# Kernel optimization log

Hardware: AMD Instinct MI355X
Metric: run time of the kernel (lower is better)

Reference implementation:

```python
import jax, jax.numpy as jnp
import numpy as np

B, T, D, H, L, W = 32, 512, 256, 8, 2, 10
NQ = 10000
HD = D // H


def setup_inputs():
    key = jax.random.key(0)
    ks = jax.random.split(key, 16)
    def n(k, shape, s=0.02):
        return jax.random.normal(k, shape, jnp.float32) * s
    return {
        "q": jax.random.randint(ks[0], (B, T), 0, NQ),
        "s": jax.random.randint(ks[1], (B, T), 0, 2),
        "q_embed": n(ks[2], (NQ + 1, D)),
        "s_embed": n(ks[3], (2, D)),
        "pos_embed": n(ks[4], (512, D)),
        "fusion_w": n(ks[5], (2 * D, D)),
        "fusion_b": jnp.zeros((D,), jnp.float32),
        "in_proj_w": n(ks[6], (L, D, 3 * D)),
        "in_proj_b": jnp.zeros((L, 3 * D), jnp.float32),
        "out_proj_w": n(ks[7], (L, D, D)),
        "out_proj_b": jnp.zeros((L, D), jnp.float32),
        "ln1_g": jnp.ones((L, D), jnp.float32),
        "ln1_b": jnp.zeros((L, D), jnp.float32),
        "ln2_g": jnp.ones((L, D), jnp.float32),
        "ln2_b": jnp.zeros((L, D), jnp.float32),
        "ff1_w": n(ks[8], (L, D, 4 * D)),
        "ff1_b": jnp.zeros((L, 4 * D), jnp.float32),
        "ff2_w": n(ks[9], (L, 4 * D, D)),
        "ff2_b": jnp.zeros((L, D), jnp.float32),
        "sw1": n(ks[10], (6, 32), 0.1),
        "sb1": jnp.zeros((32,), jnp.float32),
        "sw2": n(ks[11], (32, D // 4), 0.1),
        "sb2": jnp.zeros((D // 4,), jnp.float32),
        "cw1": n(ks[12], (D + D // 4, D)),
        "cb1": jnp.zeros((D,), jnp.float32),
        "cw2": n(ks[13], (D, 1)),
        "cb2": jnp.zeros((1,), jnp.float32),
    }


def _ln(x, g, b):
    mu = jnp.mean(x, -1, keepdims=True)
    var = jnp.mean(jnp.square(x - mu), -1, keepdims=True)
    return (x - mu) * jax.lax.rsqrt(var + 1e-5) * g + b


def _sliding_sum(x, w):
    # sum over trailing window of size w ending at each t, via prefix sums
    c = jnp.concatenate([jnp.zeros((x.shape[0], 1), x.dtype), jnp.cumsum(x, axis=1)], axis=1)
    t = jnp.arange(x.shape[1])
    return c[:, t + 1] - c[:, jnp.maximum(t + 1 - w, 0)]


def _stats(s, mask):
    # vectorized version of _extract_statistics (prefix-sum sliding windows)
    mf = mask.astype(jnp.float32)
    sf = s.astype(jnp.float32) * mf
    valid = _sliding_sum(mf, W)
    correct_rate = _sliding_sum(sf, W) / (valid + 1e-6)
    rc = _sliding_sum(mf, 5)
    recent_correct = _sliding_sum(sf, 5) / (rc + 1e-6)
    trans = ((s[:, 1:] != s[:, :-1]) & mask[:, 1:] & mask[:, :-1]).astype(jnp.float32)
    diff = jnp.concatenate([jnp.zeros((s.shape[0], 1), jnp.float32), trans], axis=1)
    change_rate = _sliding_sum(diff, W - 1) / (valid + 1e-6)
    # max consecutive equal run within each trailing window of size W
    sp = jnp.pad(s, ((0, 0), (W - 1, 0)))
    mp = jnp.pad(mask, ((0, 0), (W - 1, 0)))
    win_s = [sp[:, j:j + T] for j in range(W)]
    win_m = [mp[:, j:j + T] for j in range(W)]
    run = win_m[0].astype(jnp.float32)
    mx = run
    for j in range(1, W):  # fixed small window, not a data-dim loop
        eq = (win_s[j] == win_s[j - 1]) & win_m[j - 1]
        run = win_m[j].astype(jnp.float32) * (jnp.where(eq, run, 0.0) + 1.0)
        mx = jnp.maximum(mx, run)
    rel = jnp.broadcast_to(jnp.arange(T, dtype=jnp.float32) / max(T, 100), s.shape)
    cov = valid / W
    return jnp.stack([correct_rate, recent_correct, change_rate, mx / W, rel, cov], axis=-1)


def reference(q, s, q_embed, s_embed, pos_embed, fusion_w, fusion_b, in_proj_w, in_proj_b,
              out_proj_w, out_proj_b, ln1_g, ln1_b, ln2_g, ln2_b, ff1_w, ff1_b, ff2_w, ff2_b,
              sw1, sb1, sw2, sb2, cw1, cb1, cw2, cb2):
    mask = s >= 0
    qm = jnp.where(mask, q, 0)
    sm = jnp.where(mask, s, 0)
    h = jnp.concatenate([q_embed[qm], s_embed[sm]], axis=-1)  # [B,T,2D]
    h = jax.nn.relu(h @ fusion_w + fusion_b) + pos_embed[:T][None]
    causal = jnp.tril(jnp.ones((T, T), bool))
    allowed = causal[None, None] & mask[:, None, None, :]
    scale = 1.0 / (HD ** 0.5)
    for l in range(L):
        qkv = h @ in_proj_w[l] + in_proj_b[l]
        qh, kh, vh = jnp.split(qkv, 3, axis=-1)
        qh = qh.reshape(B, T, H, HD).transpose(0, 2, 1, 3)
        kh = kh.reshape(B, T, H, HD).transpose(0, 2, 1, 3)
        vh = vh.reshape(B, T, H, HD).transpose(0, 2, 1, 3)
        scores = jnp.einsum('bhqd,bhkd->bhqk', qh, kh) * scale
        scores = jnp.where(allowed, scores, -1e9)
        attn = jax.nn.softmax(scores, axis=-1)
        o = jnp.einsum('bhqk,bhkd->bhqd', attn, vh).transpose(0, 2, 1, 3).reshape(B, T, D)
        h = _ln(h + (o @ out_proj_w[l] + out_proj_b[l]), ln1_g[l], ln1_b[l])
        ff = jax.nn.gelu(h @ ff1_w[l] + ff1_b[l], approximate=False) @ ff2_w[l] + ff2_b[l]
        h = _ln(h + ff, ln2_g[l], ln2_b[l])
    sfeat = _stats(sm, mask)  # [B,T,6]
    semb = jax.nn.relu(sfeat @ sw1 + sb1) @ sw2 + sb2  # [B,T,D//4]
    comb = jnp.concatenate([h, semb], axis=-1)
    logits = (jax.nn.relu(comb @ cw1 + cb1) @ cw2 + cb2)[..., 0]
    return jnp.where(mask, logits, -1e9)
```

## Files before the change

kernel.cpp:

```cpp
#include <hip/hip_runtime.h>
#include <hip/hip_bf16.h>
#include <cmath>


using short8 = __attribute__((ext_vector_type(8))) short;
using short4v = __attribute__((ext_vector_type(4))) short;
using f32x4  = __attribute__((ext_vector_type(4))) float;

__device__ inline float gelu_f(float x) {
    return 0.5f * x * (1.0f + erff(x * 0.70710678118654752f));
}

__device__ inline short f2bf(float x) {
    union { float f; unsigned u; } v; v.f = x;
    return (short)((v.u + 0x7fffu + ((v.u >> 16) & 1u)) >> 16);
}

__device__ inline float bf2f(short v) {
    union { unsigned u; float f; } x; x.u = ((unsigned)(unsigned short)v) << 16;
    return x.f;
}

__device__ inline unsigned packbf(float lo, float hi) {
    union { float f; unsigned u; } a, b; a.f = lo; b.f = hi;
    unsigned ra = (a.u + 0x7fffu + ((a.u >> 16) & 1u)) >> 16;
    unsigned rb = (b.u + 0x7fffu + ((b.u >> 16) & 1u)) >> 16;
    return (rb << 16) | (ra & 0xffffu);
}

#define GLOAD16(gp, lp) __builtin_amdgcn_global_load_lds( \
    (const __attribute__((address_space(1))) void*)(gp), \
    (__attribute__((address_space(3))) void*)(lp), 16, 0, 0)

__global__ __launch_bounds__(256) void prep(
    const float* __restrict__ fusion_w, const float* __restrict__ in_proj_w,
    const float* __restrict__ out_proj_w, const float* __restrict__ ff1_w,
    const float* __restrict__ ff2_w, const float* __restrict__ cw1,
    short* __restrict__ wts,
    const int* __restrict__ s,
    short* __restrict__ semb,
    const float* __restrict__ sw1, const float* __restrict__ sb1,
    const float* __restrict__ sw2, const float* __restrict__ sb2)
{
    __shared__ float tile[4][32][33];
    __shared__ float sv_sh[512];
    __shared__ float m_sh[512];
    __shared__ float sw2_sh[2048];

    if (blockIdx.x < 436) {
        const int b0[10]      = {0,128,320,512,576,640,896,1152,1408,1664};
        const int Ks[10]      = {512,256,256,256,256,256,256,1024,1024,320};
        const int Ns[10]      = {256,768,768,256,256,1024,1024,256,256,256};
        const int sidx[10]    = {0,1,1,2,2,3,3,4,4,5};
        const size_t soff[10] = {0,0,196608,0,65536,0,262144,0,262144,0};
        const size_t doff[10] = {0,131072,327680,524288,589824,655360,917504,1179648,1441792,1703936};
        const float* srcs[6] = {fusion_w, in_proj_w, out_proj_w, ff1_w, ff2_w, cw1};
        const int c = threadIdx.x & 31, r = threadIdx.x >> 5;

        int mis[4], txs[4], tys[4];
#pragma unroll
        for (int i = 0; i < 4; ++i) {
            int tg = blockIdx.x * 4 + i;
            int mi = 0;
            while (mi < 9 && tg >= b0[mi + 1]) ++mi;
            int bl = tg - b0[mi];
            mis[i] = mi;
            txs[i] = bl % (Ns[mi] >> 5);
            tys[i] = bl / (Ns[mi] >> 5);
        }
#pragma unroll
        for (int i = 0; i < 4; ++i) {
            const float* src = srcs[sidx[mis[i]]] + soff[mis[i]];
            const int N = Ns[mis[i]];
#pragma unroll
            for (int u = 0; u < 4; ++u)
                tile[i][r + u * 8][c] =
                    src[(size_t)(tys[i] * 32 + r + u * 8) * N + txs[i] * 32 + c];
        }
        __syncthreads();
#pragma unroll
        for (int i = 0; i < 4; ++i) {
            short* dst = wts + doff[mis[i]];
            const int K = Ks[mis[i]];
#pragma unroll
            for (int u = 0; u < 4; ++u)
                dst[(size_t)(txs[i] * 32 + r + u * 8) * K + tys[i] * 32 + c] =
                    f2bf(tile[i][c][r + u * 8]);
        }
    } else {
        const int b = blockIdx.x - 436;
        const int tt = threadIdx.x;
        for (int t = tt; t < 512; t += 256) {
            int sval = s[b * 512 + t];
            bool mk = sval >= 0;
            sv_sh[t] = mk ? (float)sval : 0.f;
            m_sh[t] = mk ? 1.f : 0.f;
        }
        for (int i = tt; i < 2048; i += 256) sw2_sh[i] = sw2[i];
        __syncthreads();
        for (int half = 0; half < 2; ++half) {
            const int t = tt + half * 256;
            float mf10 = 0, sf10 = 0, mf5 = 0, sf5 = 0, d9 = 0;
#pragma unroll
            for (int k = 0; k < 10; ++k) {
                int idx = t - k;
                if (idx >= 0) {
                    float mv = m_sh[idx], sv = sv_sh[idx];
                    mf10 += mv; sf10 += sv;
                    if (k < 5) { mf5 += mv; sf5 += sv; }
                    if (k < 9 && idx >= 1) {
                        if (sv != sv_sh[idx - 1] && mv > 0.5f && m_sh[idx - 1] > 0.5f) d9 += 1.f;
                    }
                }
            }
            float run, mx;
            {
                int x0 = t - 9;
                run = (x0 >= 0) ? m_sh[x0] : 0.f;
                mx = run;
#pragma unroll
                for (int j = 1; j < 10; ++j) {
                    int xc = t + j - 9, xp = xc - 1;
                    float sc = (xc >= 0) ? sv_sh[xc] : 0.f;
                    float sp = (xp >= 0) ? sv_sh[xp] : 0.f;
                    float mc = (xc >= 0) ? m_sh[xc] : 0.f;
                    float mp = (xp >= 0) ? m_sh[xp] : 0.f;
                    bool eq = (sc == sp) && (mp > 0.5f);
                    run = (mc > 0.5f) ? ((eq ? run : 0.f) + 1.f) : 0.f;
                    mx = fmaxf(mx, run);
                }
            }
            float f[6];
            f[0] = sf10 / (mf10 + 1e-6f);
            f[1] = sf5 / (mf5 + 1e-6f);
            f[2] = d9 / (mf10 + 1e-6f);
            f[3] = mx * 0.1f;
            f[4] = (float)t * (1.f / 512.f);
            f[5] = mf10 * 0.1f;

            float hid[32];
#pragma unroll
            for (int j2 = 0; j2 < 32; ++j2) {
                float a = sb1[j2];
#pragma unroll
                for (int i = 0; i < 6; ++i) a = fmaf(f[i], sw1[i * 32 + j2], a);
                hid[j2] = fmaxf(a, 0.f);
            }
            short* orow = semb + ((size_t)b * 512 + t) * 64;
            for (int c = 0; c < 64; c += 4) {
                float v0 = sb2[c], v1 = sb2[c + 1], v2 = sb2[c + 2], v3 = sb2[c + 3];
#pragma unroll
                for (int j2 = 0; j2 < 32; ++j2) {
                    float hh = hid[j2];
                    v0 = fmaf(hh, sw2_sh[j2 * 64 + c], v0);
                    v1 = fmaf(hh, sw2_sh[j2 * 64 + c + 1], v1);
                    v2 = fmaf(hh, sw2_sh[j2 * 64 + c + 2], v2);
                    v3 = fmaf(hh, sw2_sh[j2 * 64 + c + 3], v3);
                }
                short4v o; o[0] = f2bf(v0); o[1] = f2bf(v1); o[2] = f2bf(v2); o[3] = f2bf(v3);
                *(short4v*)(orow + c) = o;
            }
        }
    }
}

template<int EPI, int KTOT>
__global__ __launch_bounds__(512) void kbs(
    const short* __restrict__ A, const short* __restrict__ Wt,
    const float* __restrict__ bias,
    short* __restrict__ o0, short* __restrict__ o1, short* __restrict__ o2,
    const float* __restrict__ pos,
    const int* __restrict__ qi, const int* __restrict__ si,
    const float* __restrict__ qe, const float* __restrict__ se)
{
    constexpr int BN = 64;
    constexpr int NCH = (KTOT + 255) / 256;
    __shared__ short Bs[BN * 256];
    const int tid = threadIdx.x, lane = tid & 63, wv = tid >> 6;
    const int lg = lane >> 4, lr = lane & 15;
    const int n0 = blockIdx.y * BN;
    const int row0 = blockIdx.x * 128 + wv * 16;

    f32x4 acc[4] = {};
    short8 af[8];

#pragma unroll
    for (int c = 0; c < NCH; ++c) {
        const int ck = (KTOT - c * 256 >= 256) ? 256 : (KTOT - c * 256);
        const int spr = ck >> 3;
        if (c) __syncthreads();
        for (int i = 0; i < (BN * ck) / 8; i += 512) {
            int slot = i + tid;
            int n = slot / spr, posn = slot % spr;
            int g = posn ^ (n & 7);
            GLOAD16(Wt + (size_t)(n0 + n) * KTOT + c * 256 + g * 8, &Bs[slot * 8]);
        }
        const int nkk = ck >> 5;
        if constexpr (EPI == 0) {
            int row = row0 + lr;
            int sv = si[row];
            bool mk = sv >= 0;
            const float* base = (c == 0) ? qe + (size_t)(mk ? qi[row] : 0) * 256
                                         : se + (size_t)(mk ? sv : 0) * 256;
#pragma unroll
            for (int kk = 0; kk < 8; ++kk) {
                const float* p = base + kk * 32 + lg * 8;
                float4 v0 = *(const float4*)p;
                float4 v1 = *(const float4*)(p + 4);
                short8 o;
                o[0] = f2bf(v0.x); o[1] = f2bf(v0.y); o[2] = f2bf(v0.z); o[3] = f2bf(v0.w);
                o[4] = f2bf(v1.x); o[5] = f2bf(v1.y); o[6] = f2bf(v1.z); o[7] = f2bf(v1.w);
                af[kk] = o;
            }
        } else {
            const short* ar = A + (size_t)(row0 + lr) * KTOT + c * 256 + lg * 8;
#pragma unroll
            for (int kk = 0; kk < 8; ++kk)
                if (kk < nkk) af[kk] = *(const short8*)(ar + kk * 32);
        }
        __syncthreads();
#pragma unroll
        for (int kk = 0; kk < 8; ++kk) {
            if (kk >= nkk) break;
#pragma unroll
            for (int j = 0; j < 4; ++j) {
                int n = j * 16 + lr;
                short8 b = *(const short8*)&Bs[n * ck + (((kk * 4 + lg) ^ (n & 7)) << 3)];
                acc[j] = __builtin_amdgcn_mfma_f32_16x16x32_bf16(af[kk], b, acc[j], 0, 0, 0);
            }
        }
    }

    if constexpr (EPI == 0) {
#pragma unroll
        for (int j = 0; j < 4; ++j)
#pragma unroll
        for (int r = 0; r < 4; ++r) {
            int row = row0 + lg * 4 + r;
            int col = n0 + j * 16 + lr;
            float x = acc[j][r] + bias[col];
            x = fmaxf(x, 0.f) + pos[(size_t)(row & 511) * 256 + col];
            o0[(size_t)row * 256 + col] = f2bf(x);
        }
    } else if constexpr (EPI == 1) {
#pragma unroll
        for (int j = 0; j < 4; ++j)
#pragma unroll
        for (int r = 0; r < 4; ++r) {
            int row = row0 + lg * 4 + r;
            int gcol = n0 + j * 16 + lr;
            int t = row & 511, bg = row >> 9;
            int sec = gcol >> 8, cc = gcol & 255;
            int h = cc >> 5, d = cc & 31, bh = bg * 8 + h;
            short v = f2bf(acc[j][r] + bias[gcol]);
            if (sec == 0)      o0[((size_t)bh * 512 + t) * 32 + d] = v;
            else if (sec == 1) o1[((size_t)bh * 512 + t) * 32 + d] = v;
            else {
                int kl = t & 31;
                o2[(size_t)bh * 16384 + (size_t)(t >> 5) * 1024 +
                   (size_t)((kl >> 2) & 3) * 256 + d * 8 + (((kl & 3) << 1) | ((kl >> 4) & 1))] = v;
            }
        }
    } else {
#pragma unroll
        for (int j = 0; j < 4; ++j)
#pragma unroll
        for (int r = 0; r < 4; ++r) {
            int row = row0 + lg * 4 + r;
            int gcol = n0 + j * 16 + lr;
            float x = acc[j][r] + bias[gcol];
            o0[(size_t)row * 1024 + gcol] = f2bf(gelu_f(x));
        }
    }
}

template<int EPI, int KTOT>
__global__ __launch_bounds__(512) void kfull(
    const short* __restrict__ A, const short* __restrict__ A2,
    const short* __restrict__ Wt, const float* __restrict__ bias,
    short* __restrict__ hb,
    const float* __restrict__ gamma, const float* __restrict__ beta,
    const float* __restrict__ cw2v, const float* __restrict__ cb2,
    const int* __restrict__ smask, float* __restrict__ outlog)
{
    constexpr int NCH = (KTOT + 127) / 128;
    constexpr int KA = (EPI == 1) ? 256 : KTOT;
    __shared__ short Bs[256 * 128];
    __shared__ float redS[32][4];
    __shared__ float redQ[32][4];
    const int tid = threadIdx.x, lane = tid & 63, wv = tid >> 6;
    const int lg = lane >> 4, lr = lane & 15;
    const int wr = wv >> 2, wc = wv & 3;
    const int row0 = blockIdx.x * 32 + wr * 16;

    f32x4 acc[4] = {};
    short8 af[4];

#pragma unroll
    for (int c = 0; c < NCH; ++c) {
        const int ck = (KTOT - c * 128 >= 128) ? 128 : (KTOT - c * 128);
        const int spr = ck >> 3;
        if (c) __syncthreads();
        for (int i = 0; i < (256 * ck) / 8; i += 512) {
            int slot = i + tid;
            int n = slot / spr, posn = slot % spr;
            int g = posn ^ (n & 7);
            GLOAD16(Wt + (size_t)n * KTOT + c * 128 + g * 8, &Bs[slot * 8]);
        }
        const int nkk = ck >> 5;
        if (EPI == 1 && c == 2) {
            const short* ar2 = A2 + (size_t)(row0 + lr) * 64 + lg * 8;
            af[0] = *(const short8*)(ar2);
            af[1] = *(const short8*)(ar2 + 32);
        } else {
            const short* ar = A + (size_t)(row0 + lr) * KA + c * 128 + lg * 8;
#pragma unroll
            for (int kk = 0; kk < 4; ++kk)
                if (kk < nkk) af[kk] = *(const short8*)(ar + kk * 32);
        }
        __syncthreads();
#pragma unroll
        for (int kk = 0; kk < 4; ++kk) {
            if (kk >= nkk) break;
#pragma unroll
            for (int j = 0; j < 4; ++j) {
                int n = wc * 64 + j * 16 + lr;
                short8 b = *(const short8*)&Bs[n * ck + (((kk * 4 + lg) ^ (n & 7)) << 3)];
                acc[j] = __builtin_amdgcn_mfma_f32_16x16x32_bf16(af[kk], b, acc[j], 0, 0, 0);
            }
        }
    }

    if constexpr (EPI == 0) {
        float ps[4] = {0.f, 0.f, 0.f, 0.f}, pq[4] = {0.f, 0.f, 0.f, 0.f};
#pragma unroll
        for (int j = 0; j < 4; ++j)
#pragma unroll
        for (int r = 0; r < 4; ++r) {
            int row = row0 + lg * 4 + r;
            int col = wc * 64 + j * 16 + lr;
            float x = acc[j][r] + bias[col] + bf2f(hb[(size_t)row * 256 + col]);
            acc[j][r] = x;
            ps[r] += x; pq[r] += x * x;
        }
#pragma unroll
        for (int off = 1; off < 16; off <<= 1)
#pragma unroll
            for (int r = 0; r < 4; ++r) {
                ps[r] += __shfl_xor(ps[r], off);
                pq[r] += __shfl_xor(pq[r], off);
            }
        if (lr == 0) {
#pragma unroll
            for (int r = 0; r < 4; ++r) {
                int rl = wr * 16 + lg * 4 + r;
                redS[rl][wc] = ps[r]; redQ[rl][wc] = pq[r];
            }
        }
        __syncthreads();
#pragma unroll
        for (int r = 0; r < 4; ++r) {
            int rl = wr * 16 + lg * 4 + r;
            int row = row0 + lg * 4 + r;
            float sm = redS[rl][0] + redS[rl][1] + redS[rl][2] + redS[rl][3];
            float sq = redQ[rl][0] + redQ[rl][1] + redQ[rl][2] + redQ[rl][3];
            float mu = sm * (1.f / 256.f);
            float var = sq * (1.f / 256.f) - mu * mu;
            float rstd = rsqrtf(var + 1e-5f);
#pragma unroll
            for (int j = 0; j < 4; ++j) {
                int col = wc * 64 + j * 16 + lr;
                float y = (acc[j][r] - mu) * rstd * gamma[col] + beta[col];
                hb[(size_t)row * 256 + col] = f2bf(y);
            }
        }
    } else {
        float p[4] = {0.f, 0.f, 0.f, 0.f};
#pragma unroll
        for (int j = 0; j < 4; ++j)
#pragma unroll
        for (int r = 0; r < 4; ++r) {
            int col = wc * 64 + j * 16 + lr;
            float v = fmaxf(acc[j][r] + bias[col], 0.f);
            p[r] += v * cw2v[col];
        }
#pragma unroll
        for (int off = 1; off < 16; off <<= 1)
#pragma unroll
            for (int r = 0; r < 4; ++r) p[r] += __shfl_xor(p[r], off);
        if (lr == 0) {
#pragma unroll
            for (int r = 0; r < 4; ++r)
                redS[wr * 16 + lg * 4 + r][wc] = p[r];
        }
        __syncthreads();
        if (tid < 32) {
            int row = blockIdx.x * 32 + tid;
            float v = redS[tid][0] + redS[tid][1] + redS[tid][2] + redS[tid][3] + cb2[0];
            outlog[row] = (smask[row] >= 0) ? v : -1e9f;
        }
    }
}

__global__ __launch_bounds__(256) void attn_mfma(
    const short* __restrict__ Qg, const short* __restrict__ Kg,
    const short* __restrict__ VTg, short* __restrict__ O)
{
    __shared__ unsigned Wp[4][2][16][20];
    const int bh = blockIdx.x >> 2, part = blockIdx.x & 3;
    const int b = bh >> 3, h = bh & 7;
    const int wv = threadIdx.x >> 6, lane = threadIdx.x & 63;
    const int lg = lane >> 4, lr = lane & 15;
    const int slot = part * 4 + wv;
    const short* Qbh = Qg + (size_t)bh * 16384;
    const short* Kbh = Kg + (size_t)bh * 16384;
    const short* Vbh = VTg + (size_t)bh * 16384;
    const float scale = 0.17677669529663687f;

    const int tA = slot, tB = 31 - slot;
    const int qA0 = tA << 4, qB0 = tB << 4;
    const int nA = tA >> 1, nB = tB >> 1;
    short8 qaA = *(const short8*)(Qbh + (size_t)(qA0 + lr) * 32 + lg * 8);
    short8 qaB = *(const short8*)(Qbh + (size_t)(qB0 + lr) * 32 + lg * 8);
    f32x4 oA0 = {}, oA1 = {}, oB0 = {}, oB1 = {};
    float lA[4] = {0.f, 0.f, 0.f, 0.f};
    float lB[4] = {0.f, 0.f, 0.f, 0.f};

    auto chunk = [&](int c, int q0, int nfull, const short8& qa,
                     const short8& kf0, const short8& kf1,
                     const short8& vf0, const short8& vf1,
                     f32x4& o0, f32x4& o1, float* l_, int slab) {
        int kc = c << 5;
        f32x4 s0 = {}, s1 = {};
        s0 = __builtin_amdgcn_mfma_f32_16x16x32_bf16(qa, kf0, s0, 0, 0, 0);
        s1 = __builtin_amdgcn_mfma_f32_16x16x32_bf16(qa, kf1, s1, 0, 0, 0);
        float p0[4], p1[4];
        if (c < nfull) {
#pragma unroll
            for (int r = 0; r < 4; ++r) {
                p0[r] = __expf(s0[r] * scale);
                p1[r] = __expf(s1[r] * scale);
            }
        } else {
#pragma unroll
            for (int r = 0; r < 4; ++r) {
                int qq = q0 + lg * 4 + r;
                p0[r] = (kc + lr)      > qq ? 0.f : __expf(s0[r] * scale);
                p1[r] = (kc + 16 + lr) > qq ? 0.f : __expf(s1[r] * scale);
            }
        }
#pragma unroll
        for (int r = 0; r < 4; ++r) {
            l_[r] += p0[r] + p1[r];
            Wp[wv][slab][lg * 4 + r][lr] = packbf(p0[r], p1[r]);
        }
        short8 pa = *(const short8*)&Wp[wv][slab][lr][lg * 4];
        o0 = __builtin_amdgcn_mfma_f32_16x16x32_bf16(pa, vf0, o0, 0, 0, 0);
        o1 = __builtin_amdgcn_mfma_f32_16x16x32_bf16(pa, vf1, o1, 0, 0, 0);
    };

    int c = 0;
    for (; c <= nA; ++c) {
        int kc = c << 5;
        short8 kf0 = *(const short8*)(Kbh + (size_t)(kc + lr) * 32 + lg * 8);
        short8 kf1 = *(const short8*)(Kbh + (size_t)(kc + 16 + lr) * 32 + lg * 8);
        short8 vf0 = *(const short8*)(Vbh + (size_t)c * 1024 + lg * 256 + lr * 8);
        short8 vf1 = *(const short8*)(Vbh + (size_t)c * 1024 + lg * 256 + (lr + 16) * 8);
        chunk(c, qB0, nB, qaB, kf0, kf1, vf0, vf1, oB0, oB1, lB, 1);
        chunk(c, qA0, nA, qaA, kf0, kf1, vf0, vf1, oA0, oA1, lA, 0);
    }
    for (; c <= nB; ++c) {
        int kc = c << 5;
        short8 kf0 = *(const short8*)(Kbh + (size_t)(kc + lr) * 32 + lg * 8);
        short8 kf1 = *(const short8*)(Kbh + (size_t)(kc + 16 + lr) * 32 + lg * 8);
        short8 vf0 = *(const short8*)(Vbh + (size_t)c * 1024 + lg * 256 + lr * 8);
        short8 vf1 = *(const short8*)(Vbh + (size_t)c * 1024 + lg * 256 + (lr + 16) * 8);
        chunk(c, qB0, nB, qaB, kf0, kf1, vf0, vf1, oB0, oB1, lB, 1);
    }

#pragma unroll
    for (int off = 1; off < 16; off <<= 1)
#pragma unroll
        for (int r = 0; r < 4; ++r) {
            lA[r] += __shfl_xor(lA[r], off);
            lB[r] += __shfl_xor(lB[r], off);
        }
#pragma unroll
    for (int r = 0; r < 4; ++r) {
        float invA = 1.f / lA[r];
        size_t roA = ((size_t)b * 512 + qA0 + lg * 4 + r) * 256 + h * 32;
        O[roA + lr] = f2bf(oA0[r] * invA);
        O[roA + 16 + lr] = f2bf(oA1[r] * invA);
        float invB = 1.f / lB[r];
        size_t roB = ((size_t)b * 512 + qB0 + lg * 4 + r) * 256 + h * 32;
        O[roB + lr] = f2bf(oB0[r] * invB);
        O[roB + 16 + lr] = f2bf(oB1[r] * invB);
    }
}

extern "C" void kernel_launch(void* const* d_in, const int* in_sizes, int n_in,
                              void* d_out, int out_size, void* d_ws, size_t ws_size,
                              hipStream_t stream) {
    const int*   q         = (const int*)d_in[0];
    const int*   s         = (const int*)d_in[1];
    const float* q_embed   = (const float*)d_in[2];
    const float* s_embed   = (const float*)d_in[3];
    const float* pos_embed = (const float*)d_in[4];
    const float* fusion_w  = (const float*)d_in[5];
    const float* fusion_b  = (const float*)d_in[6];
    const float* in_proj_w = (const float*)d_in[7];
    const float* in_proj_b = (const float*)d_in[8];
    const float* out_proj_w= (const float*)d_in[9];
    const float* out_proj_b= (const float*)d_in[10];
    const float* ln1_g     = (const float*)d_in[11];
    const float* ln1_b     = (const float*)d_in[12];
    const float* ln2_g     = (const float*)d_in[13];
    const float* ln2_b     = (const float*)d_in[14];
    const float* ff1_w     = (const float*)d_in[15];
    const float* ff1_b     = (const float*)d_in[16];
    const float* ff2_w     = (const float*)d_in[17];
    const float* ff2_b     = (const float*)d_in[18];
    const float* sw1       = (const float*)d_in[19];
    const float* sb1       = (const float*)d_in[20];
    const float* sw2       = (const float*)d_in[21];
    const float* sb2       = (const float*)d_in[22];
    const float* cw1       = (const float*)d_in[23];
    const float* cb1       = (const float*)d_in[24];
    const float* cw2       = (const float*)d_in[25];
    const float* cb2       = (const float*)d_in[26];
    float* out = (float*)d_out;

    char* base = (char*)d_ws;
    short* hb   = (short*)(base);
    short* bufA = (short*)(base + 8388608);
    short* att  = (short*)(base + 41943040);
    short* Qg   = (short*)(base + 50331648);
    short* Kg   = (short*)(base + 58720256);
    short* VTg  = (short*)(base + 67108864);
    short* semb = (short*)(base + 75497472);
    short* wts  = (short*)(base + 77594624);

    const size_t W_FUSION = 0, W_INPROJ0 = 131072, W_INPROJ1 = 327680;
    const size_t W_OUTPROJ0 = 524288, W_OUTPROJ1 = 589824;
    const size_t W_FF1_0 = 655360, W_FF1_1 = 917504;
    const size_t W_FF2_0 = 1179648, W_FF2_1 = 1441792;
    const size_t W_CW1 = 1703936;

    prep<<<468, 256, 0, stream>>>(fusion_w, in_proj_w, out_proj_w,
                                  ff1_w, ff2_w, cw1, wts,
                                  s, semb, sw1, sb1, sw2, sb2);
    kbs<0, 512><<<dim3(128, 4), 512, 0, stream>>>(nullptr,
        wts + W_FUSION, fusion_b, hb, nullptr, nullptr,
        pos_embed, q, s, q_embed, s_embed);
    for (int l = 0; l < 2; ++l) {
        kbs<1, 256><<<dim3(128, 12), 512, 0, stream>>>(hb,
            wts + (l ? W_INPROJ1 : W_INPROJ0), in_proj_b + l * 768,
            Qg, Kg, VTg, nullptr, nullptr, nullptr, nullptr, nullptr);
        attn_mfma<<<1024, 256, 0, stream>>>(Qg, Kg, VTg, att);
        kfull<0, 256><<<512, 512, 0, stream>>>(att, nullptr,
            wts + (l ? W_OUTPROJ1 : W_OUTPROJ0), out_proj_b + l * 256,
            hb, ln1_g + l * 256, ln1_b + l * 256,
            nullptr, nullptr, nullptr, nullptr);
        kbs<2, 256><<<dim3(128, 16), 512, 0, stream>>>(hb,
            wts + (l ? W_FF1_1 : W_FF1_0), ff1_b + l * 1024,
            bufA, nullptr, nullptr, nullptr, nullptr, nullptr, nullptr, nullptr);
        kfull<0, 1024><<<512, 512, 0, stream>>>(bufA, nullptr,
            wts + (l ? W_FF2_1 : W_FF2_0), ff2_b + l * 256,
            hb, ln2_g + l * 256, ln2_b + l * 256,
            nullptr, nullptr, nullptr, nullptr);
    }
    kfull<1, 320><<<512, 512, 0, stream>>>(hb, semb,
        wts + W_CW1, cb1, nullptr, nullptr, nullptr,
        cw2, cb2, s, out);
}
```

Before: 275.4 us.

## Fuse attention with out-projection, residual add and LayerNorm in one kernel

The separate attention kernel and the out-projection+LN kernel are merged. Each block now handles one batch and one 16-row query tile across all 8 heads, with one wave per head. Attention output is staged in swizzled LDS and multiplied by Wo via MFMA, then the residual and bias are added and LayerNorm is applied with a cross-wave reduction. This removes the att buffer round trip and a kernel launch. The trade-off is that the earlier balanced pairing of short and long causal tiles is dropped, so blocks with late query tiles do much more work than early ones, and every block reloads the full Wo matrix from global memory.

```diff
diff --git a/kernel.cpp b/kernel.cpp
--- a/kernel.cpp
+++ b/kernel.cpp
@@ -402,35 +402,35 @@
     }
 }
 
-__global__ __launch_bounds__(256) void attn_mfma(
+__global__ __launch_bounds__(512) void attn_oln(
     const short* __restrict__ Qg, const short* __restrict__ Kg,
-    const short* __restrict__ VTg, short* __restrict__ O)
+    const short* __restrict__ VTg, const short* __restrict__ Wo,
+    const float* __restrict__ ob, short* __restrict__ hb,
+    const float* __restrict__ gamma, const float* __restrict__ beta)
 {
-    __shared__ unsigned Wp[4][2][16][20];
-    const int bh = blockIdx.x >> 2, part = blockIdx.x & 3;
-    const int b = bh >> 3, h = bh & 7;
-    const int wv = threadIdx.x >> 6, lane = threadIdx.x & 63;
+    __shared__ unsigned Wp[8][16][20];
+    __shared__ short att_sh[16][256];
+    __shared__ float redS[16][8];
+    __shared__ float redQ[16][8];
+    const int b = blockIdx.x >> 5, qt = blockIdx.x & 31;
+    const int h = threadIdx.x >> 6, lane = threadIdx.x & 63;
     const int lg = lane >> 4, lr = lane & 15;
-    const int slot = part * 4 + wv;
+    const int bh = b * 8 + h;
     const short* Qbh = Qg + (size_t)bh * 16384;
     const short* Kbh = Kg + (size_t)bh * 16384;
     const short* Vbh = VTg + (size_t)bh * 16384;
     const float scale = 0.17677669529663687f;
-
-    const int tA = slot, tB = 31 - slot;
-    const int qA0 = tA << 4, qB0 = tB << 4;
-    const int nA = tA >> 1, nB = tB >> 1;
-    short8 qaA = *(const short8*)(Qbh + (size_t)(qA0 + lr) * 32 + lg * 8);
-    short8 qaB = *(const short8*)(Qbh + (size_t)(qB0 + lr) * 32 + lg * 8);
-    f32x4 oA0 = {}, oA1 = {}, oB0 = {}, oB1 = {};
-    float lA[4] = {0.f, 0.f, 0.f, 0.f};
-    float lB[4] = {0.f, 0.f, 0.f, 0.f};
-
-    auto chunk = [&](int c, int q0, int nfull, const short8& qa,
-                     const short8& kf0, const short8& kf1,
-                     const short8& vf0, const short8& vf1,
-                     f32x4& o0, f32x4& o1, float* l_, int slab) {
+    const int q0 = qt << 4;
+    const int nfull = qt >> 1;
+
+    short8 qa = *(const short8*)(Qbh + (size_t)(q0 + lr) * 32 + lg * 8);
+    f32x4 o0 = {}, o1 = {};
+    float l_[4] = {0.f, 0.f, 0.f, 0.f};
+
+    for (int c = 0; c <= nfull; ++c) {
         int kc = c << 5;
+        short8 kf0 = *(const short8*)(Kbh + (size_t)(kc + lr) * 32 + lg * 8);
+        short8 kf1 = *(const short8*)(Kbh + (size_t)(kc + 16 + lr) * 32 + lg * 8);
         f32x4 s0 = {}, s1 = {};
         s0 = __builtin_amdgcn_mfma_f32_16x16x32_bf16(qa, kf0, s0, 0, 0, 0);
         s1 = __builtin_amdgcn_mfma_f32_16x16x32_bf16(qa, kf1, s1, 0, 0, 0);
@@ -452,49 +452,86 @@
 #pragma unroll
         for (int r = 0; r < 4; ++r) {
             l_[r] += p0[r] + p1[r];
-            Wp[wv][slab][lg * 4 + r][lr] = packbf(p0[r], p1[r]);
-        }
-        short8 pa = *(const short8*)&Wp[wv][slab][lr][lg * 4];
+            Wp[h][lg * 4 + r][lr] = packbf(p0[r], p1[r]);
+        }
+        short8 pa = *(const short8*)&Wp[h][lr][lg * 4];
+        short8 vf0 = *(const short8*)(Vbh + (size_t)c * 1024 + lg * 256 + lr * 8);
+        short8 vf1 = *(const short8*)(Vbh + (size_t)c * 1024 + lg * 256 + (lr + 16) * 8);
         o0 = __builtin_amdgcn_mfma_f32_16x16x32_bf16(pa, vf0, o0, 0, 0, 0);
         o1 = __builtin_amdgcn_mfma_f32_16x16x32_bf16(pa, vf1, o1, 0, 0, 0);
-    };
-
-    int c = 0;
-    for (; c <= nA; ++c) {
-        int kc = c << 5;
-        short8 kf0 = *(const short8*)(Kbh + (size_t)(kc + lr) * 32 + lg * 8);
-        short8 kf1 = *(const short8*)(Kbh + (size_t)(kc + 16 + lr) * 32 + lg * 8);
-        short8 vf0 = *(const short8*)(Vbh + (size_t)c * 1024 + lg * 256 + lr * 8);
-        short8 vf1 = *(const short8*)(Vbh + (size_t)c * 1024 + lg * 256 + (lr + 16) * 8);
-        chunk(c, qB0, nB, qaB, kf0, kf1, vf0, vf1, oB0, oB1, lB, 1);
-        chunk(c, qA0, nA, qaA, kf0, kf1, vf0, vf1, oA0, oA1, lA, 0);
-    }
-    for (; c <= nB; ++c) {
-        int kc = c << 5;
-        short8 kf0 = *(const short8*)(Kbh + (size_t)(kc + lr) * 32 + lg * 8);
-        short8 kf1 = *(const short8*)(Kbh + (size_t)(kc + 16 + lr) * 32 + lg * 8);
-        short8 vf0 = *(const short8*)(Vbh + (size_t)c * 1024 + lg * 256 + lr * 8);
-        short8 vf1 = *(const short8*)(Vbh + (size_t)c * 1024 + lg * 256 + (lr + 16) * 8);
-        chunk(c, qB0, nB, qaB, kf0, kf1, vf0, vf1, oB0, oB1, lB, 1);
-    }
-
+    }
 #pragma unroll
     for (int off = 1; off < 16; off <<= 1)
 #pragma unroll
-        for (int r = 0; r < 4; ++r) {
-            lA[r] += __shfl_xor(lA[r], off);
-            lB[r] += __shfl_xor(lB[r], off);
-        }
+        for (int r = 0; r < 4; ++r) l_[r] += __shfl_xor(l_[r], off);
+
 #pragma unroll
     for (int r = 0; r < 4; ++r) {
-        float invA = 1.f / lA[r];
-        size_t roA = ((size_t)b * 512 + qA0 + lg * 4 + r) * 256 + h * 32;
-        O[roA + lr] = f2bf(oA0[r] * invA);
-        O[roA + 16 + lr] = f2bf(oA1[r] * invA);
-        float invB = 1.f / lB[r];
-        size_t roB = ((size_t)b * 512 + qB0 + lg * 4 + r) * 256 + h * 32;
-        O[roB + lr] = f2bf(oB0[r] * invB);
-        O[roB + 16 + lr] = f2bf(oB1[r] * invB);
+        float inv = 1.f / l_[r];
+        int rr = lg * 4 + r;
+        int c0 = h * 32 + lr;
+        int c1 = h * 32 + 16 + lr;
+        att_sh[rr][((((c0 >> 3) ^ (rr & 7)) << 3) | (c0 & 7))] = f2bf(o0[r] * inv);
+        att_sh[rr][((((c1 >> 3) ^ (rr & 7)) << 3) | (c1 & 7))] = f2bf(o1[r] * inv);
+    }
+    __syncthreads();
+
+    short8 af[8];
+#pragma unroll
+    for (int kk = 0; kk < 8; ++kk)
+        af[kk] = *(const short8*)&att_sh[lr][(((kk * 4 + lg) ^ (lr & 7)) << 3)];
+    f32x4 acc[2] = {};
+#pragma unroll
+    for (int kk = 0; kk < 8; ++kk)
+#pragma unroll
+    for (int j = 0; j < 2; ++j) {
+        int n = h * 32 + j * 16 + lr;
+        short8 bfr = *(const short8*)(Wo + (size_t)n * 256 + kk * 32 + lg * 8);
+        acc[j] = __builtin_amdgcn_mfma_f32_16x16x32_bf16(af[kk], bfr, acc[j], 0, 0, 0);
+    }
+
+    float xs[2][4], ps[4] = {}, pq[4] = {};
+#pragma unroll
+    for (int j = 0; j < 2; ++j)
+#pragma unroll
+    for (int r = 0; r < 4; ++r) {
+        int rr = lg * 4 + r;
+        int row = b * 512 + q0 + rr;
+        int col = h * 32 + j * 16 + lr;
+        float x = acc[j][r] + ob[col] + bf2f(hb[(size_t)row * 256 + col]);
+        xs[j][r] = x; ps[r] += x; pq[r] += x * x;
+    }
+#pragma unroll
+    for (int off = 1; off < 16; off <<= 1)
+#pragma unroll
+        for (int r = 0; r < 4; ++r) {
+            ps[r] += __shfl_xor(ps[r], off);
+            pq[r] += __shfl_xor(pq[r], off);
+        }
+    if (lr == 0) {
+#pragma unroll
+        for (int r = 0; r < 4; ++r) {
+            redS[lg * 4 + r][h] = ps[r];
+            redQ[lg * 4 + r][h] = pq[r];
+        }
+    }
+    __syncthreads();
+#pragma unroll
+    for (int r = 0; r < 4; ++r) {
+        int rr = lg * 4 + r;
+        int row = b * 512 + q0 + rr;
+        float sm = 0.f, sq = 0.f;
+#pragma unroll
+        for (int u = 0; u < 8; ++u) { sm += redS[rr][u]; sq += redQ[rr][u]; }
+        float mu = sm * (1.f / 256.f);
+        float var = sq * (1.f / 256.f) - mu * mu;
+        float rstd = rsqrtf(var + 1e-5f);
+#pragma unroll
+        for (int j = 0; j < 2; ++j) {
+            int col = h * 32 + j * 16 + lr;
+            float y = (xs[j][r] - mu) * rstd * gamma[col] + beta[col];
+            hb[(size_t)row * 256 + col] = f2bf(y);
+        }
     }
 }
 
@@ -533,12 +570,11 @@
     char* base = (char*)d_ws;
     short* hb   = (short*)(base);
     short* bufA = (short*)(base + 8388608);
-    short* att  = (short*)(base + 41943040);
-    short* Qg   = (short*)(base + 50331648);
-    short* Kg   = (short*)(base + 58720256);
-    short* VTg  = (short*)(base + 67108864);
-    short* semb = (short*)(base + 75497472);
-    short* wts  = (short*)(base + 77594624);
+    short* Qg   = (short*)(base + 41943040);
+    short* Kg   = (short*)(base + 50331648);
+    short* VTg  = (short*)(base + 58720256);
+    short* semb = (short*)(base + 67108864);
+    short* wts  = (short*)(base + 69206016);
 
     const size_t W_FUSION = 0, W_INPROJ0 = 131072, W_INPROJ1 = 327680;
     const size_t W_OUTPROJ0 = 524288, W_OUTPROJ1 = 589824;
@@ -556,11 +592,9 @@
         kbs<1, 256><<<dim3(128, 12), 512, 0, stream>>>(hb,
             wts + (l ? W_INPROJ1 : W_INPROJ0), in_proj_b + l * 768,
             Qg, Kg, VTg, nullptr, nullptr, nullptr, nullptr, nullptr);
-        attn_mfma<<<1024, 256, 0, stream>>>(Qg, Kg, VTg, att);
-        kfull<0, 256><<<512, 512, 0, stream>>>(att, nullptr,
+        attn_oln<<<1024, 512, 0, stream>>>(Qg, Kg, VTg,
             wts + (l ? W_OUTPROJ1 : W_OUTPROJ0), out_proj_b + l * 256,
-            hb, ln1_g + l * 256, ln1_b + l * 256,
-            nullptr, nullptr, nullptr, nullptr);
+            hb, ln1_g + l * 256, ln1_b + l * 256);
         kbs<2, 256><<<dim3(128, 16), 512, 0, stream>>>(hb,
             wts + (l ? W_FF1_1 : W_FF1_0), ff1_b + l * 1024,
             bufA, nullptr, nullptr, nullptr, nullptr, nullptr, nullptr, nullptr);
```

New measurement: 308.6 us. +12.0%, slower.
